# Kernel tuning notes

Measured on AMD Instinct MI355X. Metric: run time of the kernel, lower is better.

## Reference

```python
import jax, jax.numpy as jnp
from jax import lax
import numpy as np

PCR0, PCR1 = -25.6, -25.6      # point_cloud_range x/y mins
VOXX, VOXY = 0.1, 0.1          # voxel_size x/y
STRIDE = 8.0                   # bev_stride
EPS = 1e-5
RADII = dict(raw=(0.4, 0.8), c1=(0.4, 0.8), c2=(0.8, 1.2), c3=(1.2, 2.4), c4=(2.4, 4.8))
NSAMP = dict(raw=(16, 16), c1=(16, 16), c2=(16, 32), c3=(16, 32), c4=(16, 32))


def ball_query(xyz, new_xyz, radius, nsample):
    # xyz [N,3], new_xyz [M,3] -> idx [M,nsample] (first-in-index-order in-radius pts), empty mask [M]
    d2 = jnp.sum((new_xyz[:, None, :] - xyz[None, :, :]) ** 2, axis=-1)  # [M,N]
    N = xyz.shape[0]
    score = jnp.where(d2 < radius * radius, jnp.arange(N, dtype=jnp.int32)[None, :], N)
    idx = -lax.top_k(-score, nsample)[0]          # ascending: smallest valid indices first
    valid = idx < N
    first = jnp.where(valid[:, :1], idx[:, :1], 0)
    idx = jnp.where(valid, idx, first)            # duplicate first neighbor into empty slots
    return idx, ~valid[:, 0]


def mlp_bn_relu(x, W, gb):
    # shared Conv2d(1x1,bias=False)+BN2d(train stats)+ReLU over [M,S,Cin]
    h = jnp.einsum('msc,cd->msd', x, W)
    mu = h.mean(axis=(0, 1))
    var = h.var(axis=(0, 1))
    return jax.nn.relu((h - mu) * lax.rsqrt(var + EPS) * gb[0] + gb[1])


def sa_module(xyz, feats, new_xyz, radii, nsamples, W0, W1, gb0, gb1):
    # StackSAModuleMSG: per radius scale -> ball query, group xyz offsets [+feats], 2-layer MLP, max-pool
    outs = []
    for s in range(2):
        idx, empty = ball_query(xyz, new_xyz, radii[s], nsamples[s])
        g = xyz[idx] - new_xyz[:, None, :]                       # [M,S,3]
        if feats is not None:
            g = jnp.concatenate([g, feats[idx]], axis=-1)        # [M,S,3+C]
        g = jnp.where(empty[:, None, None], 0.0, g)              # empty_ball_mask -> zeros
        h = mlp_bn_relu(g, W0[s], gb0[s])
        h = mlp_bn_relu(h, W1[s], gb1[s])
        outs.append(jnp.max(h, axis=1))                          # max_pool over neighbors
    return jnp.concatenate(outs, axis=-1)


def bev_interp(bev, kp):
    # exact port of bilinear_interpolate_torch; bev [H,W,C], kp [M,3] -> [M,C]
    x = (kp[:, 0] - PCR0) / VOXX / STRIDE
    y = (kp[:, 1] - PCR1) / VOXY / STRIDE
    H, W = bev.shape[0], bev.shape[1]
    x0 = jnp.floor(x).astype(jnp.int32); x1 = x0 + 1
    y0 = jnp.floor(y).astype(jnp.int32); y1 = y0 + 1
    x0 = jnp.clip(x0, 0, W - 1); x1 = jnp.clip(x1, 0, W - 1)
    y0 = jnp.clip(y0, 0, H - 1); y1 = jnp.clip(y1, 0, H - 1)
    Ia, Ib, Ic, Id = bev[y0, x0], bev[y1, x0], bev[y0, x1], bev[y1, x1]
    wa = (x1 - x) * (y1 - y); wb = (x1 - x) * (y - y0)
    wc = (x - x0) * (y1 - y); wd = (x - x0) * (y - y0)
    return Ia * wa[:, None] + Ib * wb[:, None] + Ic * wc[:, None] + Id * wd[:, None]


def _forward(kp, raw_xyz, bev, c1_xyz, c1_feat, c2_xyz, c2_feat, c3_xyz, c3_feat, c4_xyz, c4_feat,
             raw_W0, raw_W1, raw_gb0, raw_gb1, c1_W0, c1_W1, c1_gb0, c1_gb1,
             c2_W0, c2_W1, c2_gb0, c2_gb1, c3_W0, c3_W1, c3_gb0, c3_gb1,
             c4_W0, c4_W1, c4_gb0, c4_gb1, fus_W, fus_gb):
    fl = [bev_interp(bev, kp)]
    fl.append(sa_module(raw_xyz, None, kp, RADII['raw'], NSAMP['raw'], raw_W0, raw_W1, raw_gb0, raw_gb1))
    for name, x, f, W0, W1, g0, g1 in [
            ('c1', c1_xyz, c1_feat, c1_W0, c1_W1, c1_gb0, c1_gb1),
            ('c2', c2_xyz, c2_feat, c2_W0, c2_W1, c2_gb0, c2_gb1),
            ('c3', c3_xyz, c3_feat, c3_W0, c3_W1, c3_gb0, c3_gb1),
            ('c4', c4_xyz, c4_feat, c4_W0, c4_W1, c4_gb0, c4_gb1)]:
        fl.append(sa_module(x, f, kp, RADII[name], NSAMP[name], W0, W1, g0, g1))
    h = jnp.concatenate(fl, axis=-1) @ fus_W        # [M,512] @ [512,32]
    mu = h.mean(axis=0); var = h.var(axis=0)        # Linear(bias=False)+BN1d+ReLU fusion
    return jax.nn.relu((h - mu) * lax.rsqrt(var + EPS) * fus_gb[0] + fus_gb[1])


def setup_inputs() -> dict:
    keys = iter(jax.random.split(jax.random.key(0), 80))
    lo = jnp.array([-25.6, -25.6, -2.0], jnp.float32)
    span = jnp.array([51.2, 51.2, 4.0], jnp.float32)

    def pts(n):
        return lo + span * jax.random.uniform(next(keys), (n, 3), dtype=jnp.float32)

    def w(*shape):
        return jax.random.normal(next(keys), shape, dtype=jnp.float32) / np.sqrt(shape[-2])

    def gb(c):
        g = 1.0 + 0.1 * jax.random.normal(next(keys), (2, c), dtype=jnp.float32)
        b = 0.1 * jax.random.normal(next(keys), (2, c), dtype=jnp.float32)
        return jnp.stack([g, b], axis=1)  # [scale, gamma/beta, C]

    def feat(n, c):
        return jax.random.normal(next(keys), (n, c), dtype=jnp.float32)

    return dict(
        kp=pts(2048), raw_xyz=pts(30000),
        bev=jax.random.normal(next(keys), (64, 64, 128), dtype=jnp.float32),
        c1_xyz=pts(30000), c1_feat=feat(30000, 16),
        c2_xyz=pts(16000), c2_feat=feat(16000, 32),
        c3_xyz=pts(8000), c3_feat=feat(8000, 64),
        c4_xyz=pts(4000), c4_feat=feat(4000, 64),
        raw_W0=w(2, 3, 16), raw_W1=w(2, 16, 16), raw_gb0=gb(16), raw_gb1=gb(16),
        c1_W0=w(2, 19, 16), c1_W1=w(2, 16, 16), c1_gb0=gb(16), c1_gb1=gb(16),
        c2_W0=w(2, 35, 32), c2_W1=w(2, 32, 32), c2_gb0=gb(32), c2_gb1=gb(32),
        c3_W0=w(2, 67, 64), c3_W1=w(2, 64, 64), c3_gb0=gb(64), c3_gb1=gb(64),
        c4_W0=w(2, 67, 64), c4_W1=w(2, 64, 64), c4_gb0=gb(64), c4_gb1=gb(64),
        fus_W=w(512, 32),
        fus_gb=jnp.stack([1.0 + 0.1 * jax.random.normal(next(keys), (32,), dtype=jnp.float32),
                          0.1 * jax.random.normal(next(keys), (32,), dtype=jnp.float32)]),
    )


def reference(kp, raw_xyz, bev, c1_xyz, c1_feat, c2_xyz, c2_feat, c3_xyz, c3_feat, c4_xyz, c4_feat,
              raw_W0, raw_W1, raw_gb0, raw_gb1, c1_W0, c1_W1, c1_gb0, c1_gb1,
              c2_W0, c2_W1, c2_gb0, c2_gb1, c3_W0, c3_W1, c3_gb0, c3_gb1,
              c4_W0, c4_W1, c4_gb0, c4_gb1, fus_W, fus_gb):
    return _forward(kp, raw_xyz, bev, c1_xyz, c1_feat, c2_xyz, c2_feat, c3_xyz, c3_feat, c4_xyz, c4_feat,
                    raw_W0, raw_W1, raw_gb0, raw_gb1, c1_W0, c1_W1, c1_gb0, c1_gb1,
                    c2_W0, c2_W1, c2_gb0, c2_gb1, c3_W0, c3_W1, c3_gb0, c3_gb1,
                    c4_W0, c4_W1, c4_gb0, c4_gb1, fus_W, fus_gb)
```

## Files before the change

### kernel.cpp

```cpp
#include <hip/hip_runtime.h>
#include <math.h>

#define DEV_INLINE __device__ __forceinline__

struct Cfg {
  const float* xyz;
  const float* feat;
  const float* W0;
  const float* W1;
  const float* gb0;
  const float* gb1;
  int N, S, Cfeat, C0;
  int logS, logC0;
  int colOff;
  int idxOff;
  int emptyOff;
  int statOff;
  int mmOff;
  int hIdxOff;
  int bncOff;
  int h0Off;
  float r2;
};
struct AllCfg { Cfg c[10]; };

struct PairCfg {
  int N, ptsOff;
  float r2s, r2b;
  int S0, S1;
  int hIdxOff0, hIdxOff1;
  int ci0, ci1;
};
struct PairAll { PairCfg p[5]; };

struct PackCfg { const float* src; int N; int off; };
struct PackAll { PackCfg c[5]; };

static const int M = 2048;

DEV_INLINE unsigned fkey(float f) {
  unsigned u = __float_as_uint(f);
  return (u & 0x80000000u) ? ~u : (u | 0x80000000u);
}
DEV_INLINE float funkey(unsigned k) {
  return __uint_as_float((k & 0x80000000u) ? (k & 0x7fffffffu) : ~k);
}

DEV_INLINE void decode_tile(int b, int& ci, int& t) {
  if (b < 1536) {
    const int m = b % 3;
    ci = (m == 0) ? 5 : ((m == 1) ? 7 : 9);
    t = 512 + b / 3;
  } else {
    b -= 1536;
    ci = b % 10;
    t = b / 10;
  }
}

__global__ __launch_bounds__(256) void k_pack(PackAll pk, float4* __restrict__ pts4) {
  const PackCfg c = pk.c[blockIdx.y];
  const int j = blockIdx.x * 256 + threadIdx.x;
  if (j >= c.N) return;
  pts4[c.off + j] = make_float4(c.src[3 * j], c.src[3 * j + 1], c.src[3 * j + 2], 0.f);
}

__global__ __launch_bounds__(256) void k_ballq3(PairAll pairs, const float* __restrict__ kp,
                                                const float4* __restrict__ pts4,
                                                unsigned short* __restrict__ hidx,
                                                int* __restrict__ hcnt) {
  const PairCfg pc = pairs.p[blockIdx.y];
  const int lane = threadIdx.x & 63;
  const int wave = threadIdx.x >> 6;
  const int w = blockIdx.x * 4 + wave;
  const int seg = w >> 8;
  const int kbase = (w & 255) * 8;
  const int N = pc.N;
  const int Nq = ((N / 4 + 63) / 64) * 64;
  const int start = seg * Nq;
  const int end = min(N, start + Nq);
  const float4* __restrict__ pts = pts4 + pc.ptsOff;
  const float r2s = pc.r2s, r2b = pc.r2b;
  const int S0 = pc.S0, S1 = pc.S1;
  const unsigned long long lt = (1ull << lane) - 1ull;

  float qx[8], qy[8], qz[8];
  int cnt0[8], cnt1[8];
  #pragma unroll
  for (int k = 0; k < 8; ++k) {
    qx[k] = kp[(kbase + k) * 3 + 0];
    qy[k] = kp[(kbase + k) * 3 + 1];
    qz[k] = kp[(kbase + k) * 3 + 2];
    cnt0[k] = 0; cnt1[k] = 0;
  }

  unsigned short* outA = hidx + pc.hIdxOff0 + (seg * 2048 + kbase) * S0;
  unsigned short* outB = hidx + pc.hIdxOff1 + (seg * 2048 + kbase) * S1;
// ... 166 lines not shown
    constexpr int CF4 = (CIN - 3) / 4;
    const float4* f4 = (const float4*)cfg.feat + (size_t)idx * CF4;
    for (int c = j; c < CF4; c += 4) {
      float4 v;
      if (emp) v = make_float4(0.f, 0.f, 0.f, 0.f); else v = f4[c];
      dst[3 + 4 * c] = v.x; dst[4 + 4 * c] = v.y;
      dst[5 + 4 * c] = v.z; dst[6 + 4 * c] = v.w;
    }
  }
}

__global__ __launch_bounds__(64) void k_bnc(AllCfg cfgs, const double* __restrict__ statsR,
                                            float* __restrict__ bnc, int phase) {
  const Cfg cfg = cfgs.c[blockIdx.x];
  const int cc = threadIdx.x;
  if (cc >= cfg.C0) return;
  const int off = cfg.statOff + (phase ? 128 : 0);
  double s = 0.0, q = 0.0;
  #pragma unroll
  for (int r = 0; r < 4; ++r) {
    s += statsR[r * 2560 + off + cc];
    q += statsR[r * 2560 + off + 64 + cc];
  }
  const double n = (double)(2048 * cfg.S);
  const double mu = s / n;
  const double var = q / n - mu * mu;
  const double inv = 1.0 / sqrt(var + 1e-5);
  const float* gb = phase ? cfg.gb1 : cfg.gb0;
  const double g = (double)gb[cc], b = (double)gb[cfg.C0 + cc];
  bnc[cfg.bncOff + cc] = (float)(inv * g);
  bnc[cfg.bncOff + 64 + cc] = (float)(b - mu * inv * g);
}

template<int C0, int CIN, int S>
__device__ __forceinline__ void p1_impl(const Cfg& cfg, const float* __restrict__ kp,
                                        const unsigned short* __restrict__ idxbuf,
                                        const int* __restrict__ emptybuf,
                                        double* __restrict__ statsR,
                                        float* __restrict__ h0g, int tile, char* smem) {
  constexpr int CPD = CIN + 1;
  constexpr int CPR = (C0 == 16) ? 20 : (CPD > C0 ? CPD : C0);
  constexpr int NCG = C0 / 4;
  constexpr int RPT = NCG / 4;
  constexpr int RPTc = (RPT < 1) ? 1 : RPT;
  constexpr int LOGCG = (NCG == 4) ? 2 : ((NCG == 8) ? 3 : 4);
  float* in_f = (float*)smem;
  const int tid = threadIdx.x;
  stage_rows2<CIN, S, CPR>(cfg, kp, idxbuf, emptybuf, tile * 64, in_f);
  const int cg = tid & (NCG - 1);
  const int rg = tid >> LOGCG;
  const int r0 = rg * RPTc;
  const int cc0 = 4 * cg;
  __syncthreads();
  float acc[RPTc][4];
  #pragma unroll
  for (int rr = 0; rr < RPTc; ++rr)
    acc[rr][0] = acc[rr][1] = acc[rr][2] = acc[rr][3] = 0.f;
  const float* W0g = cfg.W0 + cc0;
  #pragma unroll 2
  for (int c4 = 0; c4 < CIN / 4; ++c4) {
    const float4 w0 = *(const float4*)(W0g + (4 * c4 + 0) * C0);
    const float4 w1 = *(const float4*)(W0g + (4 * c4 + 1) * C0);
    const float4 w2 = *(const float4*)(W0g + (4 * c4 + 2) * C0);
    const float4 w3 = *(const float4*)(W0g + (4 * c4 + 3) * C0);
    #pragma unroll
    for (int rr = 0; rr < RPTc; ++rr) {
      const float4 a = *(const float4*)(in_f + (r0 + rr) * CPR + 4 * c4);
      acc[rr][0] += a.x * w0.x + a.y * w1.x + a.z * w2.x + a.w * w3.x;
      acc[rr][1] += a.x * w0.y + a.y * w1.y + a.z * w2.y + a.w * w3.y;
      acc[rr][2] += a.x * w0.z + a.y * w1.z + a.z * w2.z + a.w * w3.z;
      acc[rr][3] += a.x * w0.w + a.y * w1.w + a.z * w2.w + a.w * w3.w;
    }
  }
  {
    constexpr int ci0 = (CIN / 4) * 4;
    const float4 w0 = *(const float4*)(W0g + (ci0 + 0) * C0);
    const float4 w1 = *(const float4*)(W0g + (ci0 + 1) * C0);
    const float4 w2 = *(const float4*)(W0g + (ci0 + 2) * C0);
    #pragma unroll
    for (int rr = 0; rr < RPTc; ++rr) {
      const float4 a = *(const float4*)(in_f + (r0 + rr) * CPR + ci0);
      acc[rr][0] += a.x * w0.x + a.y * w1.x + a.z * w2.x;
      acc[rr][1] += a.x * w0.y + a.y * w1.y + a.z * w2.y;
      acc[rr][2] += a.x * w0.z + a.y * w1.z + a.z * w2.z;
      acc[rr][3] += a.x * w0.w + a.y * w1.w + a.z * w2.w;
    }
  }
  if (h0g) {
    float* dst = h0g + cfg.h0Off;
    #pragma unroll
    for (int rr = 0; rr < RPTc; ++rr) {
      float4 o;
      o.x = acc[rr][0]; o.y = acc[rr][1]; o.z = acc[rr][2]; o.w = acc[rr][3];
      *(float4*)(dst + (size_t)(tile * 64 + r0 + rr) * C0 + cc0) = o;
    }
  }
  float ls[4], lq[4];
  #pragma unroll
  for (int cj = 0; cj < 4; ++cj) {
    float s = 0.f, q = 0.f;
    #pragma unroll
    for (int rr = 0; rr < RPTc; ++rr) { s += acc[rr][cj]; q += acc[rr][cj] * acc[rr][cj]; }
    ls[cj] = s; lq[cj] = q;
  }
  __syncthreads();
  float* sA = (float*)smem;
  float* sB = sA + 64;
  #pragma unroll
  for (int cj = 0; cj < 4; ++cj)
    #pragma unroll
    for (int off = NCG; off < 64; off <<= 1) {
      ls[cj] += __shfl_xor(ls[cj], off);
      lq[cj] += __shfl_xor(lq[cj], off);
    }
  if (tid < 64) { sA[tid] = 0.f; sB[tid] = 0.f; }
  __syncthreads();
  if ((tid & 63) < NCG) {
    #pragma unroll
    for (int cj = 0; cj < 4; ++cj) {
      atomicAdd(&sA[cc0 + cj], ls[cj]);
      atomicAdd(&sB[cc0 + cj], lq[cj]);
    }
  }
  __syncthreads();
  const int rep = blockIdx.x & 3;
  if (tid < C0) {
    atomicAdd(&statsR[rep * 2560 + cfg.statOff + tid], (double)sA[tid]);
    atomicAdd(&statsR[rep * 2560 + cfg.statOff + 64 + tid], (double)sB[tid]);
  }
}

__global__ __launch_bounds__(256) void k_p1_all(AllCfg cfgs, const float* __restrict__ kp,
                                                const unsigned short* __restrict__ idxbuf,
                                                const int* __restrict__ emptybuf,
                                                double* __restrict__ statsR,
                                                float* __restrict__ h0g) {
  __shared__ char smem[17408];
  int ci, t;
  decode_tile(blockIdx.x, ci, t);
  switch (ci) {
    case 0: p1_impl<16, 3, 16>(cfgs.c[0], kp, idxbuf, emptybuf, statsR, h0g, t, smem); break;
    case 1: p1_impl<16, 3, 16>(cfgs.c[1], kp, idxbuf, emptybuf, statsR, h0g, t, smem); break;
    case 2: p1_impl<16, 19, 16>(cfgs.c[2], kp, idxbuf, emptybuf, statsR, h0g, t, smem); break;
    case 3: p1_impl<16, 19, 16>(cfgs.c[3], kp, idxbuf, emptybuf, statsR, h0g, t, smem); break;
    case 4: p1_impl<32, 35, 16>(cfgs.c[4], kp, idxbuf, emptybuf, statsR, h0g, t, smem); break;
    case 5: p1_impl<32, 35, 32>(cfgs.c[5], kp, idxbuf, emptybuf, statsR, h0g, t, smem); break;
    case 6: p1_impl<64, 67, 16>(cfgs.c[6], kp, idxbuf, emptybuf, statsR, h0g, t, smem); break;
    case 7: p1_impl<64, 67, 32>(cfgs.c[7], kp, idxbuf, emptybuf, statsR, h0g, t, smem); break;
    case 8: p1_impl<64, 67, 16>(cfgs.c[8], kp, idxbuf, emptybuf, statsR, h0g, t, smem); break;
    case 9: p1_impl<64, 67, 32>(cfgs.c[9], kp, idxbuf, emptybuf, statsR, h0g, t, smem); break;
  }
}

template<int C0, int S>
__device__ __forceinline__ void p2b_impl(const Cfg& cfg, const float* __restrict__ h0g,
                                         double* __restrict__ statsR,
                                         const float* __restrict__ bnc0,
                                         float* __restrict__ maxbuf,
                                         float* __restrict__ minbuf, int tile, char* smem) {
  constexpr int NCG = C0 / 4;
  constexpr int RPT = (NCG / 4 < 1) ? 1 : NCG / 4;
  constexpr int CPR = C0 + 4;
  constexpr int LOGCG = (NCG == 4) ? 2 : ((NCG == 8) ? 3 : 4);
  constexpr int LOGS = (S == 16) ? 4 : 5;
  constexpr int NM = 64 / S;
  constexpr int RPP = 256 >> LOGCG;
  constexpr int NPASS = 64 / RPP;
  float* a0 = (float*)smem;
  unsigned* mxl = (unsigned*)(smem + 17408);
  unsigned* mnl = mxl + 256;
  const int tid = threadIdx.x;
  const int cg = tid & (NCG - 1);
  const int rg = tid >> LOGCG;
  const int cc0 = 4 * cg;
  if (tid < NM * C0) { mxl[tid] = 0u; mnl[tid] = 0xFFFFFFFFu; }
  {
    const float4 scv = *(const float4*)(bnc0 + cfg.bncOff + cc0);
    const float4 shv = *(const float4*)(bnc0 + cfg.bncOff + 64 + cc0);
    const float* src = h0g + cfg.h0Off + (size_t)tile * 64 * C0;
    #pragma unroll
    for (int p = 0; p < NPASS; ++p) {
      const int row = rg + p * RPP;
      const float4 v = *(const float4*)(src + (size_t)row * C0 + cc0);
      float4 o;
      o.x = fmaxf(v.x * scv.x + shv.x, 0.f);
      o.y = fmaxf(v.y * scv.y + shv.y, 0.f);
      o.z = fmaxf(v.z * scv.z + shv.z, 0.f);
      o.w = fmaxf(v.w * scv.w + shv.w, 0.f);
      *(float4*)(a0 + row * CPR + cc0) = o;
    }
  }
  __syncthreads();
  const int r0 = rg * RPT;
  float acc1[RPT][4];
  #pragma unroll
  for (int rr = 0; rr < RPT; ++rr)
    acc1[rr][0] = acc1[rr][1] = acc1[rr][2] = acc1[rr][3] = 0.f;
  const float* W1g = cfg.W1 + cc0;
  #pragma unroll 2
  for (int c4 = 0; c4 < C0 / 4; ++c4) {
    const float4 w0 = *(const float4*)(W1g + (4 * c4 + 0) * C0);
    const float4 w1 = *(const float4*)(W1g + (4 * c4 + 1) * C0);
    const float4 w2 = *(const float4*)(W1g + (4 * c4 + 2) * C0);
    const float4 w3 = *(const float4*)(W1g + (4 * c4 + 3) * C0);
    #pragma unroll
    for (int rr = 0; rr < RPT; ++rr) {
      const float4 a = *(const float4*)(a0 + (r0 + rr) * CPR + 4 * c4);
      acc1[rr][0] += a.x * w0.x + a.y * w1.x + a.z * w2.x + a.w * w3.x;
      acc1[rr][1] += a.x * w0.y + a.y * w1.y + a.z * w2.y + a.w * w3.y;
      acc1[rr][2] += a.x * w0.z + a.y * w1.z + a.z * w2.z + a.w * w3.z;
      acc1[rr][3] += a.x * w0.w + a.y * w1.w + a.z * w2.w + a.w * w3.w;
    }
  }
  float ls[4], lq[4];
  #pragma unroll
  for (int cj = 0; cj < 4; ++cj) {
    float s = 0.f, q = 0.f;
    unsigned kmax = 0u, kmin = 0xFFFFFFFFu;
    #pragma unroll
    for (int rr = 0; rr < RPT; ++rr) {
      const float v = acc1[rr][cj];
      s += v; q += v * v;
      const unsigned kk = fkey(v);
      kmax = kmax > kk ? kmax : kk;
      kmin = kmin < kk ? kmin : kk;
    }
    ls[cj] = s; lq[cj] = q;
    const int cell = (r0 >> LOGS) * C0 + cc0 + cj;
    atomicMax(&mxl[cell], kmax);
    atomicMin(&mnl[cell], kmin);
  }
  __syncthreads();
  float* sA = (float*)smem;
  float* sB = sA + 64;
  #pragma unroll
  for (int cj = 0; cj < 4; ++cj)
    #pragma unroll
    for (int off = NCG; off < 64; off <<= 1) {
      ls[cj] += __shfl_xor(ls[cj], off);
      lq[cj] += __shfl_xor(lq[cj], off);
    }
  if (tid < 64) { sA[tid] = 0.f; sB[tid] = 0.f; }
  __syncthreads();
  if ((tid & 63) < NCG) {
    #pragma unroll
    for (int cj = 0; cj < 4; ++cj) {
      atomicAdd(&sA[cc0 + cj], ls[cj]);
      atomicAdd(&sB[cc0 + cj], lq[cj]);
    }
  }
  __syncthreads();
  const int rep = blockIdx.x & 3;
  if (tid < C0) {
    atomicAdd(&statsR[rep * 2560 + cfg.statOff + 128 + tid], (double)sA[tid]);
    atomicAdd(&statsR[rep * 2560 + cfg.statOff + 192 + tid], (double)sB[tid]);
  }
  __syncthreads();
  if (tid < NM * C0) {
    const int gcell = ((tile * 64) >> LOGS) * C0 + tid;
    maxbuf[cfg.mmOff + gcell] = funkey(mxl[tid]);
    minbuf[cfg.mmOff + gcell] = funkey(mnl[tid]);
  }
}

__global__ __launch_bounds__(256) void k_p2b_all(AllCfg cfgs, const float* __restrict__ h0g,
                                                 double* __restrict__ statsR,
                                                 const float* __restrict__ bnc0,
                                                 float* __restrict__ maxbuf,
                                                 float* __restrict__ minbuf) {
  __shared__ char smem[17408 + 2048];
  int ci, t;
  decode_tile(blockIdx.x, ci, t);
  switch (ci) {
    case 0: p2b_impl<16, 16>(cfgs.c[0], h0g, statsR, bnc0, maxbuf, minbuf, t, smem); break;
    case 1: p2b_impl<16, 16>(cfgs.c[1], h0g, statsR, bnc0, maxbuf, minbuf, t, smem); break;
    case 2: p2b_impl<16, 16>(cfgs.c[2], h0g, statsR, bnc0, maxbuf, minbuf, t, smem); break;
    case 3: p2b_impl<16, 16>(cfgs.c[3], h0g, statsR, bnc0, maxbuf, minbuf, t, smem); break;
    case 4: p2b_impl<32, 16>(cfgs.c[4], h0g, statsR, bnc0, maxbuf, minbuf, t, smem); break;
    case 5: p2b_impl<32, 32>(cfgs.c[5], h0g, statsR, bnc0, maxbuf, minbuf, t, smem); break;
    case 6: p2b_impl<64, 16>(cfgs.c[6], h0g, statsR, bnc0, maxbuf, minbuf, t, smem); break;
    case 7: p2b_impl<64, 32>(cfgs.c[7], h0g, statsR, bnc0, maxbuf, minbuf, t, smem); break;
    case 8: p2b_impl<64, 16>(cfgs.c[8], h0g, statsR, bnc0, maxbuf, minbuf, t, smem); break;
    case 9: p2b_impl<64, 32>(cfgs.c[9], h0g, statsR, bnc0, maxbuf, minbuf, t, smem); break;
  }
}

template<int C0, int CIN, int S>
__device__ __forceinline__ void p2_impl(const Cfg& cfg, const float* __restrict__ kp,
                                        const unsigned short* __restrict__ idxbuf,
                                        const int* __restrict__ emptybuf,
                                        double* __restrict__ statsR,
                                        const float* __restrict__ bnc0,
                                        float* __restrict__ maxbuf,
                                        float* __restrict__ minbuf, int tile, char* smem) {
  constexpr int CPD = CIN + 1;
  constexpr int CPR = (C0 == 16) ? 20 : (CPD > C0 ? CPD : C0);
  constexpr int NCG = C0 / 4;
  constexpr int RPT = NCG / 4;
  constexpr int RPTc = (RPT < 1) ? 1 : RPT;
  constexpr int LOGCG = (NCG == 4) ? 2 : ((NCG == 8) ? 3 : 4);
  constexpr int LOGS = (S == 16) ? 4 : 5;
  constexpr int NM = 64 / S;
  float* in_f = (float*)smem;
  unsigned* mxl = (unsigned*)(smem + 17408);
  unsigned* mnl = mxl + 256;
  const int tid = threadIdx.x;
  stage_rows2<CIN, S, CPR>(cfg, kp, idxbuf, emptybuf, tile * 64, in_f);
  if (tid < NM * C0) { mxl[tid] = 0u; mnl[tid] = 0xFFFFFFFFu; }
  const int cg = tid & (NCG - 1);
  const int rg = tid >> LOGCG;
  const int r0 = rg * RPTc;
  const int cc0 = 4 * cg;
  __syncthreads();
  float acc[RPTc][4];
  #pragma unroll
  for (int rr = 0; rr < RPTc; ++rr)
// ... 361 lines not shown
extern "C" void kernel_launch(void* const* d_in, const int* in_sizes, int n_in,
                              void* d_out, int out_size, void* d_ws, size_t ws_size,
                              hipStream_t stream) {
  (void)in_sizes; (void)n_in; (void)out_size;

  const float* kp   = (const float*)d_in[0];
  const float* raw  = (const float*)d_in[1];
  const float* bev  = (const float*)d_in[2];
  const float* c1x  = (const float*)d_in[3];
  const float* c1f  = (const float*)d_in[4];
  const float* c2x  = (const float*)d_in[5];
  const float* c2f  = (const float*)d_in[6];
  const float* c3x  = (const float*)d_in[7];
  const float* c3f  = (const float*)d_in[8];
  const float* c4x  = (const float*)d_in[9];
  const float* c4f  = (const float*)d_in[10];
  const float* fusW = (const float*)d_in[31];
  const float* fgb  = (const float*)d_in[32];

  char* ws = (char*)d_ws;
  double* stats = (double*)ws;
  float* bnc0   = (float*)(ws + 21504);
  float* bnc1   = (float*)(ws + 26624);
  unsigned short* idxbuf = (unsigned short*)(ws + 32768);
  int* emptybuf = (int*)(ws + 32768 + 1310720);
  float* fused  = (float*)(ws + 1425408);
  double* statsR = (double*)(ws + 1425408 + 4194304);
  float* hbuf   = (float*)(ws + 1425408 + 4194304);
  float* maxbuf = (float*)(ws + 5881856);
  float* minbuf = (float*)(ws + 9027584);
  float4* pts4  = (float4*)(ws + 12173312);
  int* hcnt = (int*)(ws + 5881856);
  unsigned short* hidx = (unsigned short*)(ws + 5881856 + 327680);
  float* h0buf = (float*)(ws + 13581312);
  const size_t need_old = 5881856;
  const size_t need_new = 12173312;
  const size_t need_bq2 = 13581312;
  const size_t need_h0  = 13581312 + 71303168ull;
  if (ws_size < need_old) return;
  const bool fast = (ws_size >= need_new);
  const bool bq3 = (ws_size >= need_bq2) && fast;
  const bool h0p = (ws_size >= need_h0) && bq3;

  AllCfg cfgs;
  int mmCum = 0, hCum = 0, h0Cum = 0;
  auto setCfg = [&](int i, const float* xyz, const float* feat, int N, int Cf, int C0, int S,
                    double r, const float* W0b, const float* W1b, const float* g0b,
                    const float* g1b, int sIdx, int col) {
    Cfg& c = cfgs.c[i];
    const int Cin = 3 + Cf;
    c.xyz = xyz; c.feat = feat;
    c.W0 = W0b + (size_t)sIdx * Cin * C0;
    c.W1 = W1b + (size_t)sIdx * C0 * C0;
    c.gb0 = g0b + (size_t)sIdx * 2 * C0;
    c.gb1 = g1b + (size_t)sIdx * 2 * C0;
    c.N = N; c.S = S; c.Cfeat = Cf; c.C0 = C0;
    c.logS = (S == 16) ? 4 : 5;
    c.logC0 = (C0 == 16) ? 4 : ((C0 == 32) ? 5 : 6);
    c.colOff = col;
    c.idxOff = i * 65536;
    c.emptyOff = i * 2048;
    c.statOff = i * 256;
    c.mmOff = mmCum;
    mmCum += 2048 * C0;
    c.hIdxOff = hCum;
    hCum += 4 * 2048 * S;
    c.bncOff = i * 128;
    c.h0Off = h0Cum;
    h0Cum += 2048 * S * C0;
    c.r2 = (float)(r * r);
  };

  const float* rW0 = (const float*)d_in[11]; const float* rW1 = (const float*)d_in[12];
  const float* rg0 = (const float*)d_in[13]; const float* rg1 = (const float*)d_in[14];
  const float* aW0 = (const float*)d_in[15]; const float* aW1 = (const float*)d_in[16];
  const float* ag0 = (const float*)d_in[17]; const float* ag1 = (const float*)d_in[18];
  const float* bW0 = (const float*)d_in[19]; const float* bW1 = (const float*)d_in[20];
  const float* bg0 = (const float*)d_in[21]; const float* bg1 = (const float*)d_in[22];
  const float* cW0 = (const float*)d_in[23]; const float* cW1 = (const float*)d_in[24];
  const float* cg0 = (const float*)d_in[25]; const float* cg1 = (const float*)d_in[26];
  const float* dW0 = (const float*)d_in[27]; const float* dW1 = (const float*)d_in[28];
  const float* dg0 = (const float*)d_in[29]; const float* dg1 = (const float*)d_in[30];

  setCfg(0, raw, nullptr, 30000,  0, 16, 16, 0.4, rW0, rW1, rg0, rg1, 0, 128);
  setCfg(1, raw, nullptr, 30000,  0, 16, 16, 0.8, rW0, rW1, rg0, rg1, 1, 144);
  setCfg(2, c1x, c1f,     30000, 16, 16, 16, 0.4, aW0, aW1, ag0, ag1, 0, 160);
  setCfg(3, c1x, c1f,     30000, 16, 16, 16, 0.8, aW0, aW1, ag0, ag1, 1, 176);
  setCfg(4, c2x, c2f,     16000, 32, 32, 16, 0.8, bW0, bW1, bg0, bg1, 0, 192);
  setCfg(5, c2x, c2f,     16000, 32, 32, 32, 1.2, bW0, bW1, bg0, bg1, 1, 224);
  setCfg(6, c3x, c3f,      8000, 64, 64, 16, 1.2, cW0, cW1, cg0, cg1, 0, 256);
  setCfg(7, c3x, c3f,      8000, 64, 64, 32, 2.4, cW0, cW1, cg0, cg1, 1, 320);
  setCfg(8, c4x, c4f,      4000, 64, 64, 16, 2.4, dW0, dW1, dg0, dg1, 0, 384);
  setCfg(9, c4x, c4f,      4000, 64, 64, 32, 4.8, dW0, dW1, dg0, dg1, 1, 448);

  hipMemsetAsync(stats, 0, 2624 * sizeof(double), stream);
  if (fast) hipMemsetAsync(statsR, 0, 4 * 2560 * sizeof(double), stream);

  if (bq3) {
    PackAll pk;
    pk.c[0] = { raw, 30000, 0 };
    pk.c[1] = { c1x, 30000, 30000 };
    pk.c[2] = { c2x, 16000, 60000 };
    pk.c[3] = { c3x,  8000, 76000 };
    pk.c[4] = { c4x,  4000, 84000 };
    PairAll pr;
    auto setPair = [&](int p, int ci0, int ci1, int N, int off) {
      PairCfg& q = pr.p[p];
      q.N = N; q.ptsOff = off;
      q.r2s = cfgs.c[ci0].r2; q.r2b = cfgs.c[ci1].r2;
      q.S0 = cfgs.c[ci0].S;   q.S1 = cfgs.c[ci1].S;
      q.hIdxOff0 = cfgs.c[ci0].hIdxOff; q.hIdxOff1 = cfgs.c[ci1].hIdxOff;
      q.ci0 = ci0; q.ci1 = ci1;
    };
    setPair(0, 0, 1, 30000, 0);
    setPair(1, 2, 3, 30000, 30000);
    setPair(2, 4, 5, 16000, 60000);
    setPair(3, 6, 7,  8000, 76000);
    setPair(4, 8, 9,  4000, 84000);
    k_pack<<<dim3(118, 5), 256, 0, stream>>>(pk, pts4);
    k_ballq3<<<dim3(256, 5), 256, 0, stream>>>(pr, kp, pts4, hidx, hcnt);
    k_merge<<<dim3(256, 10), 256, 0, stream>>>(cfgs, hidx, hcnt, idxbuf, emptybuf);
  } else {
    k_ballq<<<dim3(512, 10), 256, 0, stream>>>(cfgs, kp, idxbuf, emptybuf);
  }

  k_bev<<<dim3(1024), 256, 0, stream>>>(kp, bev, fused);
  if (fast) {
    k_p1_all<<<dim3(6656), 256, 0, stream>>>(cfgs, kp, idxbuf, emptybuf, statsR,
                                             h0p ? h0buf : nullptr);
    k_bnc<<<dim3(10), 64, 0, stream>>>(cfgs, statsR, bnc0, 0);
    if (h0p) {
      k_p2b_all<<<dim3(6656), 256, 0, stream>>>(cfgs, h0buf, statsR, bnc0, maxbuf, minbuf);
    } else {
      k_p2_all<<<dim3(6656), 256, 0, stream>>>(cfgs, kp, idxbuf, emptybuf, statsR, bnc0, maxbuf, minbuf);
    }
    k_bnc<<<dim3(10), 64, 0, stream>>>(cfgs, statsR, bnc1, 1);
    k_fin<<<dim3(512, 10), 256, 0, stream>>>(cfgs, bnc1, maxbuf, minbuf, fused);
  } else {
    k_stats0<<<dim3(256, 10), 256, 0, stream>>>(cfgs, kp, idxbuf, emptybuf, stats);
    k_stats1<<<dim3(512, 10), 256, 0, stream>>>(cfgs, kp, idxbuf, emptybuf, stats);
    k_final<<<dim3(2048, 10), 256, 0, stream>>>(cfgs, kp, idxbuf, emptybuf, stats, fused);
  }
  k_fus_mm<<<dim3(256), 256, 0, stream>>>(fused, fusW, hbuf, stats);
  k_fus_out<<<dim3(256), 256, 0, stream>>>(hbuf, stats, fgb, (float*)d_out);
}
```

Baseline: 235.4 us.

## Precompute per-point feature projection through first-layer weights before grouping

Adds a k_feat kernel that multiplies every source point's features by the feature rows of W0 once per point, storing an N×C0 table. The first MLP layer in the stats and second-pass kernels then becomes a gather of that table plus a 3-term xyz offset product, instead of gathering raw features and doing a full CIN×C0 matmul per grouped row. This replaces the previous h0 buffer write/read path (71MB) with a much smaller table. The cost is an extra kernel, recomputation of the xyz part in both passes, and random gathers into the table, which depend on workspace size being sufficient.

```diff
diff --git a/kernel.cpp b/kernel.cpp
--- a/kernel.cpp
+++ b/kernel.cpp
@@ -19,7 +19,7 @@
   int mmOff;
   int hIdxOff;
   int bncOff;
-  int h0Off;
+  int fOff;
   float r2;
 };
 struct AllCfg { Cfg c[10]; };
@@ -35,6 +35,9 @@
 
 struct PackCfg { const float* src; int N; int off; };
 struct PackAll { PackCfg c[5]; };
+
+struct FeatCfg { const float* feat; const float* W0; int N, C0, CF, logNCG, fOff; };
+struct FeatAll { FeatCfg c[8]; };
 
 static const int M = 2048;
 
@@ -63,6 +66,25 @@
   const int j = blockIdx.x * 256 + threadIdx.x;
   if (j >= c.N) return;
   pts4[c.off + j] = make_float4(c.src[3 * j], c.src[3 * j + 1], c.src[3 * j + 2], 0.f);
+}
+
+__global__ __launch_bounds__(256) void k_feat(FeatAll fa, float* __restrict__ Fbuf) {
+  const FeatCfg c = fa.c[blockIdx.y];
+  const int NCG = c.C0 >> 2;
+  const int e = blockIdx.x * 256 + threadIdx.x;
+  if (e >= c.N * NCG) return;
+  const int j = e >> c.logNCG;
+  const int cg = e & (NCG - 1);
+  const float* fr = c.feat + (size_t)j * c.CF;
+  const float* w = c.W0 + 3 * c.C0 + 4 * cg;
+  float ax = 0.f, ay = 0.f, az = 0.f, aw = 0.f;
+  for (int ci = 0; ci < c.CF; ++ci) {
+    const float x = fr[ci];
+    const float4 wv = *(const float4*)(w + (size_t)ci * c.C0);
+    ax += x * wv.x; ay += x * wv.y; az += x * wv.z; aw += x * wv.w;
+  }
+  float4 o; o.x = ax; o.y = ay; o.z = az; o.w = aw;
+  *(float4*)(Fbuf + c.fOff + (size_t)j * c.C0 + 4 * cg) = o;
 }
 
 __global__ __launch_bounds__(256) void k_ballq3(PairAll pairs, const float* __restrict__ kp,
@@ -295,12 +317,275 @@
   bnc[cfg.bncOff + 64 + cc] = (float)(b - mu * inv * g);
 }
 
+template<int S>
+DEV_INLINE void stage_gxyz(const Cfg& cfg, const float* __restrict__ kp,
+                           const unsigned short* __restrict__ idxbuf,
+                           const int* __restrict__ emptybuf,
+                           int tile, float4* gxl, int* idxL) {
+  const int tid = threadIdx.x;
+  constexpr int LOGS = (S == 16) ? 4 : 5;
+  if (tid < 64) {
+    const int grow = tile * 64 + tid;
+    const int m = grow >> LOGS;
+    const bool emp = emptybuf[cfg.emptyOff + m] != 0;
+    const int idx = (int)idxbuf[cfg.idxOff + grow];
+    idxL[tid] = idx;
+    float4 g;
+    if (emp) { g.x = 0.f; g.y = 0.f; g.z = 0.f; g.w = 0.f; }
+    else {
+      const float* p = cfg.xyz + 3 * idx;
+      g.x = p[0] - kp[m * 3 + 0];
+      g.y = p[1] - kp[m * 3 + 1];
+      g.z = p[2] - kp[m * 3 + 2];
+      g.w = 1.f;
+    }
+    gxl[tid] = g;
+  }
+}
+
+template<int C0, int S, bool HASF>
+DEV_INLINE void p1f_impl(const Cfg& cfg, const float* __restrict__ kp,
+                         const unsigned short* __restrict__ idxbuf,
+                         const int* __restrict__ emptybuf,
+                         const float* __restrict__ Fb,
+                         double* __restrict__ statsR, int tile, char* smem) {
+  constexpr int NCG = C0 / 4;
+  constexpr int RPT = (NCG / 4 < 1) ? 1 : NCG / 4;
+  constexpr int LOGCG = (NCG == 4) ? 2 : ((NCG == 8) ? 3 : 4);
+  float4* gxl = (float4*)smem;
+  int* idxL = (int*)(smem + 1024);
+  float* sA = (float*)(smem + 1280);
+  float* sB = (float*)(smem + 1536);
+  const int tid = threadIdx.x;
+  stage_gxyz<S>(cfg, kp, idxbuf, emptybuf, tile, gxl, idxL);
+  __syncthreads();
+  const int cg = tid & (NCG - 1);
+  const int rg = tid >> LOGCG;
+  const int r0 = rg * RPT;
+  const int cc0 = 4 * cg;
+  const float4 wx = *(const float4*)(cfg.W0 + 0 * C0 + cc0);
+  const float4 wy = *(const float4*)(cfg.W0 + 1 * C0 + cc0);
+  const float4 wz = *(const float4*)(cfg.W0 + 2 * C0 + cc0);
+  float ls[4] = {0.f, 0.f, 0.f, 0.f}, lq[4] = {0.f, 0.f, 0.f, 0.f};
+  #pragma unroll
+  for (int rr = 0; rr < RPT; ++rr) {
+    const int r = r0 + rr;
+    const float4 g = gxl[r];
+    float hx = g.x * wx.x + g.y * wy.x + g.z * wz.x;
+    float hy = g.x * wx.y + g.y * wy.y + g.z * wz.y;
+    float hz = g.x * wx.z + g.y * wy.z + g.z * wz.z;
+    float hw = g.x * wx.w + g.y * wy.w + g.z * wz.w;
+    if constexpr (HASF) {
+      const float4 Fv = *(const float4*)(Fb + cfg.fOff + (size_t)idxL[r] * C0 + cc0);
+      hx += g.w * Fv.x; hy += g.w * Fv.y; hz += g.w * Fv.z; hw += g.w * Fv.w;
+    }
+    ls[0] += hx; lq[0] += hx * hx;
+    ls[1] += hy; lq[1] += hy * hy;
+    ls[2] += hz; lq[2] += hz * hz;
+    ls[3] += hw; lq[3] += hw * hw;
+  }
+  #pragma unroll
+  for (int cj = 0; cj < 4; ++cj)
+    #pragma unroll
+    for (int off = NCG; off < 64; off <<= 1) {
+      ls[cj] += __shfl_xor(ls[cj], off);
+      lq[cj] += __shfl_xor(lq[cj], off);
+    }
+  if (tid < 64) { sA[tid] = 0.f; sB[tid] = 0.f; }
+  __syncthreads();
+  if ((tid & 63) < NCG) {
+    #pragma unroll
+    for (int cj = 0; cj < 4; ++cj) {
+      atomicAdd(&sA[cc0 + cj], ls[cj]);
+      atomicAdd(&sB[cc0 + cj], lq[cj]);
+    }
+  }
+  __syncthreads();
+  const int rep = blockIdx.x & 3;
+  if (tid < C0) {
+    atomicAdd(&statsR[rep * 2560 + cfg.statOff + tid], (double)sA[tid]);
+    atomicAdd(&statsR[rep * 2560 + cfg.statOff + 64 + tid], (double)sB[tid]);
+  }
+}
+
+__global__ __launch_bounds__(256) void k_p1f_all(AllCfg cfgs, const float* __restrict__ kp,
+                                                 const unsigned short* __restrict__ idxbuf,
+                                                 const int* __restrict__ emptybuf,
+                                                 const float* __restrict__ Fb,
+                                                 double* __restrict__ statsR) {
+  __shared__ char smem[1792];
+  int ci, t;
+  decode_tile(blockIdx.x, ci, t);
+  switch (ci) {
+    case 0: p1f_impl<16, 16, false>(cfgs.c[0], kp, idxbuf, emptybuf, Fb, statsR, t, smem); break;
+    case 1: p1f_impl<16, 16, false>(cfgs.c[1], kp, idxbuf, emptybuf, Fb, statsR, t, smem); break;
+    case 2: p1f_impl<16, 16, true>(cfgs.c[2], kp, idxbuf, emptybuf, Fb, statsR, t, smem); break;
+    case 3: p1f_impl<16, 16, true>(cfgs.c[3], kp, idxbuf, emptybuf, Fb, statsR, t, smem); break;
+    case 4: p1f_impl<32, 16, true>(cfgs.c[4], kp, idxbuf, emptybuf, Fb, statsR, t, smem); break;
+    case 5: p1f_impl<32, 32, true>(cfgs.c[5], kp, idxbuf, emptybuf, Fb, statsR, t, smem); break;
+    case 6: p1f_impl<64, 16, true>(cfgs.c[6], kp, idxbuf, emptybuf, Fb, statsR, t, smem); break;
+    case 7: p1f_impl<64, 32, true>(cfgs.c[7], kp, idxbuf, emptybuf, Fb, statsR, t, smem); break;
+    case 8: p1f_impl<64, 16, true>(cfgs.c[8], kp, idxbuf, emptybuf, Fb, statsR, t, smem); break;
+    case 9: p1f_impl<64, 32, true>(cfgs.c[9], kp, idxbuf, emptybuf, Fb, statsR, t, smem); break;
+  }
+}
+
+template<int C0, int S, bool HASF>
+DEV_INLINE void p2f_impl(const Cfg& cfg, const float* __restrict__ kp,
+                         const unsigned short* __restrict__ idxbuf,
+                         const int* __restrict__ emptybuf,
+                         const float* __restrict__ Fb,
+                         double* __restrict__ statsR,
+                         const float* __restrict__ bnc0,
+                         float* __restrict__ maxbuf, float* __restrict__ minbuf,
+                         int tile, char* smem) {
+  constexpr int NCG = C0 / 4;
+  constexpr int RPT = (NCG / 4 < 1) ? 1 : NCG / 4;
+  constexpr int CPR = C0 + 4;
+  constexpr int LOGCG = (NCG == 4) ? 2 : ((NCG == 8) ? 3 : 4);
+  constexpr int LOGS = (S == 16) ? 4 : 5;
+  constexpr int NM = 64 / S;
+  float* a0 = (float*)smem;
+  float4* gxl = (float4*)(smem + 17408);
+  int* idxL = (int*)(smem + 18432);
+  unsigned* mxl = (unsigned*)(smem + 18688);
+  unsigned* mnl = (unsigned*)(smem + 19712);
+  const int tid = threadIdx.x;
+  stage_gxyz<S>(cfg, kp, idxbuf, emptybuf, tile, gxl, idxL);
+  if (tid < NM * C0) { mxl[tid] = 0u; mnl[tid] = 0xFFFFFFFFu; }
+  __syncthreads();
+  const int cg = tid & (NCG - 1);
+  const int rg = tid >> LOGCG;
+  const int r0 = rg * RPT;
+  const int cc0 = 4 * cg;
+  {
+    const float4 wx = *(const float4*)(cfg.W0 + 0 * C0 + cc0);
+    const float4 wy = *(const float4*)(cfg.W0 + 1 * C0 + cc0);
+    const float4 wz = *(const float4*)(cfg.W0 + 2 * C0 + cc0);
+    const float4 scv = *(const float4*)(bnc0 + cfg.bncOff + cc0);
+    const float4 shv = *(const float4*)(bnc0 + cfg.bncOff + 64 + cc0);
+    #pragma unroll
+    for (int rr = 0; rr < RPT; ++rr) {
+      const int r = r0 + rr;
+      const float4 g = gxl[r];
+      float hx = g.x * wx.x + g.y * wy.x + g.z * wz.x;
+      float hy = g.x * wx.y + g.y * wy.y + g.z * wz.y;
+      float hz = g.x * wx.z + g.y * wy.z + g.z * wz.z;
+      float hw = g.x * wx.w + g.y * wy.w + g.z * wz.w;
+      if constexpr (HASF) {
+        const float4 Fv = *(const float4*)(Fb + cfg.fOff + (size_t)idxL[r] * C0 + cc0);
+        hx += g.w * Fv.x; hy += g.w * Fv.y; hz += g.w * Fv.z; hw += g.w * Fv.w;
+      }
+      float4 o;
+      o.x = fmaxf(hx * scv.x + shv.x, 0.f);
+      o.y = fmaxf(hy * scv.y + shv.y, 0.f);
+      o.z = fmaxf(hz * scv.z + shv.z, 0.f);
+      o.w = fmaxf(hw * scv.w + shv.w, 0.f);
+      *(float4*)(a0 + r * CPR + cc0) = o;
+    }
+  }
+  __syncthreads();
+  float acc1[RPT][4];
+  #pragma unroll
+  for (int rr = 0; rr < RPT; ++rr)
+    acc1[rr][0] = acc1[rr][1] = acc1[rr][2] = acc1[rr][3] = 0.f;
+  const float* W1g = cfg.W1 + cc0;
+  #pragma unroll 2
+  for (int c4 = 0; c4 < C0 / 4; ++c4) {
+    const float4 w0 = *(const float4*)(W1g + (4 * c4 + 0) * C0);
+    const float4 w1 = *(const float4*)(W1g + (4 * c4 + 1) * C0);
+    const float4 w2 = *(const float4*)(W1g + (4 * c4 + 2) * C0);
+    const float4 w3 = *(const float4*)(W1g + (4 * c4 + 3) * C0);
+    #pragma unroll
+    for (int rr = 0; rr < RPT; ++rr) {
+      const float4 a = *(const float4*)(a0 + (r0 + rr) * CPR + 4 * c4);
+      acc1[rr][0] += a.x * w0.x + a.y * w1.x + a.z * w2.x + a.w * w3.x;
+      acc1[rr][1] += a.x * w0.y + a.y * w1.y + a.z * w2.y + a.w * w3.y;
+      acc1[rr][2] += a.x * w0.z + a.y * w1.z + a.z * w2.z + a.w * w3.z;
+      acc1[rr][3] += a.x * w0.w + a.y * w1.w + a.z * w2.w + a.w * w3.w;
+    }
+  }
+  float ls[4], lq[4];
+  #pragma unroll
+  for (int cj = 0; cj < 4; ++cj) {
+    float s = 0.f, q = 0.f;
+    unsigned kmax = 0u, kmin = 0xFFFFFFFFu;
+    #pragma unroll
+    for (int rr = 0; rr < RPT; ++rr) {
+      const float v = acc1[rr][cj];
+      s += v; q += v * v;
+      const unsigned kk = fkey(v);
+      kmax = kmax > kk ? kmax : kk;
+      kmin = kmin < kk ? kmin : kk;
+    }
+    ls[cj] = s; lq[cj] = q;
+    const int cell = (r0 >> LOGS) * C0 + cc0 + cj;
+    atomicMax(&mxl[cell], kmax);
+    atomicMin(&mnl[cell], kmin);
+  }
+  __syncthreads();
+  float* sA = (float*)smem;
+  float* sB = sA + 64;
+  #pragma unroll
+  for (int cj = 0; cj < 4; ++cj)
+    #pragma unroll
+    for (int off = NCG; off < 64; off <<= 1) {
+      ls[cj] += __shfl_xor(ls[cj], off);
+      lq[cj] += __shfl_xor(lq[cj], off);
+    }
+  if (tid < 64) { sA[tid] = 0.f; sB[tid] = 0.f; }
+  __syncthreads();
+  if ((tid & 63) < NCG) {
+    #pragma unroll
+    for (int cj = 0; cj < 4; ++cj) {
+      atomicAdd(&sA[cc0 + cj], ls[cj]);
+      atomicAdd(&sB[cc0 + cj], lq[cj]);
+    }
+  }
+  __syncthreads();
+  const int rep = blockIdx.x & 3;
+  if (tid < C0) {
+    atomicAdd(&statsR[rep * 2560 + cfg.statOff + 128 + tid], (double)sA[tid]);
+    atomicAdd(&statsR[rep * 2560 + cfg.statOff + 192 + tid], (double)sB[tid]);
+  }
+  __syncthreads();
+  if (tid < NM * C0) {
+    const int gcell = ((tile * 64) >> LOGS) * C0 + tid;
+    maxbuf[cfg.mmOff + gcell] = funkey(mxl[tid]);
+    minbuf[cfg.mmOff + gcell] = funkey(mnl[tid]);
+  }
+}
+
+__global__ __launch_bounds__(256) void k_p2f_all(AllCfg cfgs, const float* __restrict__ kp,
+                                                 const unsigned short* __restrict__ idxbuf,
+                                                 const int* __restrict__ emptybuf,
+                                                 const float* __restrict__ Fb,
+                                                 double* __restrict__ statsR,
+                                                 const float* __restrict__ bnc0,
+                                                 float* __restrict__ maxbuf,
+                                                 float* __restrict__ minbuf) {
+  __shared__ char smem[20736];
+  int ci, t;
+  decode_tile(blockIdx.x, ci, t);
+  switch (ci) {
+    case 0: p2f_impl<16, 16, false>(cfgs.c[0], kp, idxbuf, emptybuf, Fb, statsR, bnc0, maxbuf, minbuf, t, smem); break;
+    case 1: p2f_impl<16, 16, false>(cfgs.c[1], kp, idxbuf, emptybuf, Fb, statsR, bnc0, maxbuf, minbuf, t, smem); break;
+    case 2: p2f_impl<16, 16, true>(cfgs.c[2], kp, idxbuf, emptybuf, Fb, statsR, bnc0, maxbuf, minbuf, t, smem); break;
+    case 3: p2f_impl<16, 16, true>(cfgs.c[3], kp, idxbuf, emptybuf, Fb, statsR, bnc0, maxbuf, minbuf, t, smem); break;
+    case 4: p2f_impl<32, 16, true>(cfgs.c[4], kp, idxbuf, emptybuf, Fb, statsR, bnc0, maxbuf, minbuf, t, smem); break;
+    case 5: p2f_impl<32, 32, true>(cfgs.c[5], kp, idxbuf, emptybuf, Fb, statsR, bnc0, maxbuf, minbuf, t, smem); break;
+    case 6: p2f_impl<64, 16, true>(cfgs.c[6], kp, idxbuf, emptybuf, Fb, statsR, bnc0, maxbuf, minbuf, t, smem); break;
+    case 7: p2f_impl<64, 32, true>(cfgs.c[7], kp, idxbuf, emptybuf, Fb, statsR, bnc0, maxbuf, minbuf, t, smem); break;
+    case 8: p2f_impl<64, 16, true>(cfgs.c[8], kp, idxbuf, emptybuf, Fb, statsR, bnc0, maxbuf, minbuf, t, smem); break;
+    case 9: p2f_impl<64, 32, true>(cfgs.c[9], kp, idxbuf, emptybuf, Fb, statsR, bnc0, maxbuf, minbuf, t, smem); break;
+  }
+}
+
 template<int C0, int CIN, int S>
 __device__ __forceinline__ void p1_impl(const Cfg& cfg, const float* __restrict__ kp,
                                         const unsigned short* __restrict__ idxbuf,
                                         const int* __restrict__ emptybuf,
-                                        double* __restrict__ statsR,
-                                        float* __restrict__ h0g, int tile, char* smem) {
+                                        double* __restrict__ statsR, int tile, char* smem) {
   constexpr int CPD = CIN + 1;
   constexpr int CPR = (C0 == 16) ? 20 : (CPD > C0 ? CPD : C0);
   constexpr int NCG = C0 / 4;
@@ -349,15 +634,6 @@
       acc[rr][3] += a.x * w0.w + a.y * w1.w + a.z * w2.w;
     }
   }
-  if (h0g) {
-    float* dst = h0g + cfg.h0Off;
-    #pragma unroll
-    for (int rr = 0; rr < RPTc; ++rr) {
-      float4 o;
-      o.x = acc[rr][0]; o.y = acc[rr][1]; o.z = acc[rr][2]; o.w = acc[rr][3];
-      *(float4*)(dst + (size_t)(tile * 64 + r0 + rr) * C0 + cc0) = o;
-    }
-  }
   float ls[4], lq[4];
   #pragma unroll
   for (int cj = 0; cj < 4; ++cj) {
@@ -396,155 +672,21 @@
 __global__ __launch_bounds__(256) void k_p1_all(AllCfg cfgs, const float* __restrict__ kp,
                                                 const unsigned short* __restrict__ idxbuf,
                                                 const int* __restrict__ emptybuf,
-                                                double* __restrict__ statsR,
-                                                float* __restrict__ h0g) {
+                                                double* __restrict__ statsR) {
   __shared__ char smem[17408];
   int ci, t;
   decode_tile(blockIdx.x, ci, t);
   switch (ci) {
-    case 0: p1_impl<16, 3, 16>(cfgs.c[0], kp, idxbuf, emptybuf, statsR, h0g, t, smem); break;
-    case 1: p1_impl<16, 3, 16>(cfgs.c[1], kp, idxbuf, emptybuf, statsR, h0g, t, smem); break;
-    case 2: p1_impl<16, 19, 16>(cfgs.c[2], kp, idxbuf, emptybuf, statsR, h0g, t, smem); break;
-    case 3: p1_impl<16, 19, 16>(cfgs.c[3], kp, idxbuf, emptybuf, statsR, h0g, t, smem); break;
-    case 4: p1_impl<32, 35, 16>(cfgs.c[4], kp, idxbuf, emptybuf, statsR, h0g, t, smem); break;
-    case 5: p1_impl<32, 35, 32>(cfgs.c[5], kp, idxbuf, emptybuf, statsR, h0g, t, smem); break;
-    case 6: p1_impl<64, 67, 16>(cfgs.c[6], kp, idxbuf, emptybuf, statsR, h0g, t, smem); break;
-    case 7: p1_impl<64, 67, 32>(cfgs.c[7], kp, idxbuf, emptybuf, statsR, h0g, t, smem); break;
-    case 8: p1_impl<64, 67, 16>(cfgs.c[8], kp, idxbuf, emptybuf, statsR, h0g, t, smem); break;
-    case 9: p1_impl<64, 67, 32>(cfgs.c[9], kp, idxbuf, emptybuf, statsR, h0g, t, smem); break;
-  }
-}
-
-template<int C0, int S>
-__device__ __forceinline__ void p2b_impl(const Cfg& cfg, const float* __restrict__ h0g,
-                                         double* __restrict__ statsR,
-                                         const float* __restrict__ bnc0,
-                                         float* __restrict__ maxbuf,
-                                         float* __restrict__ minbuf, int tile, char* smem) {
-  constexpr int NCG = C0 / 4;
-  constexpr int RPT = (NCG / 4 < 1) ? 1 : NCG / 4;
-  constexpr int CPR = C0 + 4;
-  constexpr int LOGCG = (NCG == 4) ? 2 : ((NCG == 8) ? 3 : 4);
-  constexpr int LOGS = (S == 16) ? 4 : 5;
-  constexpr int NM = 64 / S;
-  constexpr int RPP = 256 >> LOGCG;
-  constexpr int NPASS = 64 / RPP;
-  float* a0 = (float*)smem;
-  unsigned* mxl = (unsigned*)(smem + 17408);
-  unsigned* mnl = mxl + 256;
-  const int tid = threadIdx.x;
-  const int cg = tid & (NCG - 1);
-  const int rg = tid >> LOGCG;
-  const int cc0 = 4 * cg;
-  if (tid < NM * C0) { mxl[tid] = 0u; mnl[tid] = 0xFFFFFFFFu; }
-  {
-    const float4 scv = *(const float4*)(bnc0 + cfg.bncOff + cc0);
-    const float4 shv = *(const float4*)(bnc0 + cfg.bncOff + 64 + cc0);
-    const float* src = h0g + cfg.h0Off + (size_t)tile * 64 * C0;
-    #pragma unroll
-    for (int p = 0; p < NPASS; ++p) {
-      const int row = rg + p * RPP;
-      const float4 v = *(const float4*)(src + (size_t)row * C0 + cc0);
-      float4 o;
-      o.x = fmaxf(v.x * scv.x + shv.x, 0.f);
-      o.y = fmaxf(v.y * scv.y + shv.y, 0.f);
-      o.z = fmaxf(v.z * scv.z + shv.z, 0.f);
-      o.w = fmaxf(v.w * scv.w + shv.w, 0.f);
-      *(float4*)(a0 + row * CPR + cc0) = o;
-    }
-  }
-  __syncthreads();
-  const int r0 = rg * RPT;
-  float acc1[RPT][4];
-  #pragma unroll
-  for (int rr = 0; rr < RPT; ++rr)
-    acc1[rr][0] = acc1[rr][1] = acc1[rr][2] = acc1[rr][3] = 0.f;
-  const float* W1g = cfg.W1 + cc0;
-  #pragma unroll 2
-  for (int c4 = 0; c4 < C0 / 4; ++c4) {
-    const float4 w0 = *(const float4*)(W1g + (4 * c4 + 0) * C0);
-    const float4 w1 = *(const float4*)(W1g + (4 * c4 + 1) * C0);
-    const float4 w2 = *(const float4*)(W1g + (4 * c4 + 2) * C0);
-    const float4 w3 = *(const float4*)(W1g + (4 * c4 + 3) * C0);
-    #pragma unroll
-    for (int rr = 0; rr < RPT; ++rr) {
-      const float4 a = *(const float4*)(a0 + (r0 + rr) * CPR + 4 * c4);
-      acc1[rr][0] += a.x * w0.x + a.y * w1.x + a.z * w2.x + a.w * w3.x;
-      acc1[rr][1] += a.x * w0.y + a.y * w1.y + a.z * w2.y + a.w * w3.y;
-      acc1[rr][2] += a.x * w0.z + a.y * w1.z + a.z * w2.z + a.w * w3.z;
-      acc1[rr][3] += a.x * w0.w + a.y * w1.w + a.z * w2.w + a.w * w3.w;
-    }
-  }
-  float ls[4], lq[4];
-  #pragma unroll
-  for (int cj = 0; cj < 4; ++cj) {
-    float s = 0.f, q = 0.f;
-    unsigned kmax = 0u, kmin = 0xFFFFFFFFu;
-    #pragma unroll
-    for (int rr = 0; rr < RPT; ++rr) {
-      const float v = acc1[rr][cj];
-      s += v; q += v * v;
-      const unsigned kk = fkey(v);
-      kmax = kmax > kk ? kmax : kk;
-      kmin = kmin < kk ? kmin : kk;
-    }
-    ls[cj] = s; lq[cj] = q;
-    const int cell = (r0 >> LOGS) * C0 + cc0 + cj;
-    atomicMax(&mxl[cell], kmax);
-    atomicMin(&mnl[cell], kmin);
-  }
-  __syncthreads();
-  float* sA = (float*)smem;
-  float* sB = sA + 64;
-  #pragma unroll
-  for (int cj = 0; cj < 4; ++cj)
-    #pragma unroll
-    for (int off = NCG; off < 64; off <<= 1) {
-      ls[cj] += __shfl_xor(ls[cj], off);
-      lq[cj] += __shfl_xor(lq[cj], off);
-    }
-  if (tid < 64) { sA[tid] = 0.f; sB[tid] = 0.f; }
-  __syncthreads();
-  if ((tid & 63) < NCG) {
-    #pragma unroll
-    for (int cj = 0; cj < 4; ++cj) {
-      atomicAdd(&sA[cc0 + cj], ls[cj]);
-      atomicAdd(&sB[cc0 + cj], lq[cj]);
-    }
-  }
-  __syncthreads();
-  const int rep = blockIdx.x & 3;
-  if (tid < C0) {
-    atomicAdd(&statsR[rep * 2560 + cfg.statOff + 128 + tid], (double)sA[tid]);
-    atomicAdd(&statsR[rep * 2560 + cfg.statOff + 192 + tid], (double)sB[tid]);
-  }
-  __syncthreads();
-  if (tid < NM * C0) {
-    const int gcell = ((tile * 64) >> LOGS) * C0 + tid;
-    maxbuf[cfg.mmOff + gcell] = funkey(mxl[tid]);
-    minbuf[cfg.mmOff + gcell] = funkey(mnl[tid]);
-  }
-}
-
-__global__ __launch_bounds__(256) void k_p2b_all(AllCfg cfgs, const float* __restrict__ h0g,
-                                                 double* __restrict__ statsR,
-                                                 const float* __restrict__ bnc0,
-                                                 float* __restrict__ maxbuf,
-                                                 float* __restrict__ minbuf) {
-  __shared__ char smem[17408 + 2048];
-  int ci, t;
-  decode_tile(blockIdx.x, ci, t);
-  switch (ci) {
-    case 0: p2b_impl<16, 16>(cfgs.c[0], h0g, statsR, bnc0, maxbuf, minbuf, t, smem); break;
-    case 1: p2b_impl<16, 16>(cfgs.c[1], h0g, statsR, bnc0, maxbuf, minbuf, t, smem); break;
-    case 2: p2b_impl<16, 16>(cfgs.c[2], h0g, statsR, bnc0, maxbuf, minbuf, t, smem); break;
-    case 3: p2b_impl<16, 16>(cfgs.c[3], h0g, statsR, bnc0, maxbuf, minbuf, t, smem); break;
-    case 4: p2b_impl<32, 16>(cfgs.c[4], h0g, statsR, bnc0, maxbuf, minbuf, t, smem); break;
-    case 5: p2b_impl<32, 32>(cfgs.c[5], h0g, statsR, bnc0, maxbuf, minbuf, t, smem); break;
-    case 6: p2b_impl<64, 16>(cfgs.c[6], h0g, statsR, bnc0, maxbuf, minbuf, t, smem); break;
-    case 7: p2b_impl<64, 32>(cfgs.c[7], h0g, statsR, bnc0, maxbuf, minbuf, t, smem); break;
-    case 8: p2b_impl<64, 16>(cfgs.c[8], h0g, statsR, bnc0, maxbuf, minbuf, t, smem); break;
-    case 9: p2b_impl<64, 32>(cfgs.c[9], h0g, statsR, bnc0, maxbuf, minbuf, t, smem); break;
+    case 0: p1_impl<16, 3, 16>(cfgs.c[0], kp, idxbuf, emptybuf, statsR, t, smem); break;
+    case 1: p1_impl<16, 3, 16>(cfgs.c[1], kp, idxbuf, emptybuf, statsR, t, smem); break;
+    case 2: p1_impl<16, 19, 16>(cfgs.c[2], kp, idxbuf, emptybuf, statsR, t, smem); break;
+    case 3: p1_impl<16, 19, 16>(cfgs.c[3], kp, idxbuf, emptybuf, statsR, t, smem); break;
+    case 4: p1_impl<32, 35, 16>(cfgs.c[4], kp, idxbuf, emptybuf, statsR, t, smem); break;
+    case 5: p1_impl<32, 35, 32>(cfgs.c[5], kp, idxbuf, emptybuf, statsR, t, smem); break;
+    case 6: p1_impl<64, 67, 16>(cfgs.c[6], kp, idxbuf, emptybuf, statsR, t, smem); break;
+    case 7: p1_impl<64, 67, 32>(cfgs.c[7], kp, idxbuf, emptybuf, statsR, t, smem); break;
+    case 8: p1_impl<64, 67, 16>(cfgs.c[8], kp, idxbuf, emptybuf, statsR, t, smem); break;
+    case 9: p1_impl<64, 67, 32>(cfgs.c[9], kp, idxbuf, emptybuf, statsR, t, smem); break;
   }
 }
 
@@ -972,18 +1114,18 @@
   float4* pts4  = (float4*)(ws + 12173312);
   int* hcnt = (int*)(ws + 5881856);
   unsigned short* hidx = (unsigned short*)(ws + 5881856 + 327680);
-  float* h0buf = (float*)(ws + 13581312);
+  float* Fbuf = (float*)(ws + 13581312);
   const size_t need_old = 5881856;
   const size_t need_new = 12173312;
   const size_t need_bq2 = 13581312;
-  const size_t need_h0  = 13581312 + 71303168ull;
+  const size_t need_F  = 13581312 + 14080000ull;
   if (ws_size < need_old) return;
   const bool fast = (ws_size >= need_new);
   const bool bq3 = (ws_size >= need_bq2) && fast;
-  const bool h0p = (ws_size >= need_h0) && bq3;
+  const bool Fp = (ws_size >= need_F) && bq3;
 
   AllCfg cfgs;
-  int mmCum = 0, hCum = 0, h0Cum = 0;
+  int mmCum = 0, hCum = 0, fCum = 0;
   auto setCfg = [&](int i, const float* xyz, const float* feat, int N, int Cf, int C0, int S,
                     double r, const float* W0b, const float* W1b, const float* g0b,
                     const float* g1b, int sIdx, int col) {
@@ -1006,8 +1148,8 @@
     c.hIdxOff = hCum;
     hCum += 4 * 2048 * S;
     c.bncOff = i * 128;
-    c.h0Off = h0Cum;
-    h0Cum += 2048 * S * C0;
+    c.fOff = (Cf > 0) ? fCum : 0;
+    if (Cf > 0) fCum += N * C0;
     c.r2 = (float)(r * r);
   };
 
@@ -1035,6 +1177,21 @@
 
   hipMemsetAsync(stats, 0, 2624 * sizeof(double), stream);
   if (fast) hipMemsetAsync(statsR, 0, 4 * 2560 * sizeof(double), stream);
+
+  if (Fp) {
+    FeatAll fa;
+    for (int k = 0; k < 8; ++k) {
+      const Cfg& c = cfgs.c[2 + k];
+      fa.c[k].feat = c.feat;
+      fa.c[k].W0 = c.W0;
+      fa.c[k].N = c.N;
+      fa.c[k].C0 = c.C0;
+      fa.c[k].CF = c.Cfeat;
+      fa.c[k].logNCG = (c.C0 == 16) ? 2 : ((c.C0 == 32) ? 3 : 4);
+      fa.c[k].fOff = c.fOff;
+    }
+    k_feat<<<dim3(500, 8), 256, 0, stream>>>(fa, Fbuf);
+  }
 
   if (bq3) {
     PackAll pk;
@@ -1066,12 +1223,13 @@
 
   k_bev<<<dim3(1024), 256, 0, stream>>>(kp, bev, fused);
   if (fast) {
-    k_p1_all<<<dim3(6656), 256, 0, stream>>>(cfgs, kp, idxbuf, emptybuf, statsR,
-                                             h0p ? h0buf : nullptr);
-    k_bnc<<<dim3(10), 64, 0, stream>>>(cfgs, statsR, bnc0, 0);
-    if (h0p) {
-      k_p2b_all<<<dim3(6656), 256, 0, stream>>>(cfgs, h0buf, statsR, bnc0, maxbuf, minbuf);
+    if (Fp) {
+      k_p1f_all<<<dim3(6656), 256, 0, stream>>>(cfgs, kp, idxbuf, emptybuf, Fbuf, statsR);
+      k_bnc<<<dim3(10), 64, 0, stream>>>(cfgs, statsR, bnc0, 0);
+      k_p2f_all<<<dim3(6656), 256, 0, stream>>>(cfgs, kp, idxbuf, emptybuf, Fbuf, statsR, bnc0, maxbuf, minbuf);
     } else {
+      k_p1_all<<<dim3(6656), 256, 0, stream>>>(cfgs, kp, idxbuf, emptybuf, statsR);
+      k_bnc<<<dim3(10), 64, 0, stream>>>(cfgs, statsR, bnc0, 0);
       k_p2_all<<<dim3(6656), 256, 0, stream>>>(cfgs, kp, idxbuf, emptybuf, statsR, bnc0, maxbuf, minbuf);
     }
     k_bnc<<<dim3(10), 64, 0, stream>>>(cfgs, statsR, bnc1, 1);
```

Result: faster. 228.4 us (-3.0%).
